# Kernel tuning notes

Measured on AMD Instinct MI355X. Metric: run time of the kernel, lower is better.

Reference implementation:

```python
import jax, jax.numpy as jnp
import numpy as np

HEADS = 12
DIM_HEAD = 64
SCALE = DIM_HEAD ** -0.5


def _layer_norm(x, w):
    # LayerNorm with learned weight and zero bias (bias is a frozen zeros buffer)
    mu = jnp.mean(x, axis=-1, keepdims=True)
    var = jnp.var(x, axis=-1, keepdims=True)
    return (x - mu) * jax.lax.rsqrt(var + 1e-5) * w


def setup_inputs() -> dict:
    key = jax.random.key(0)
    ks = jax.random.split(key, 6)
    b, n, j, dim = 4, 2048, 2048, 768
    inner = HEADS * DIM_HEAD  # 768
    return {
        "x": jax.random.normal(ks[0], (b, n, dim), dtype=jnp.float32),
        "context": jax.random.normal(ks[1], (b, j, dim), dtype=jnp.float32),
        "mask": jnp.zeros((b, n, j), dtype=jnp.float32),
        "ln_w": jnp.ones((dim,), dtype=jnp.float32),
        "Wq": jax.random.normal(ks[2], (dim, inner), dtype=jnp.float32) * (dim ** -0.5),
        "Wkv": jax.random.normal(ks[3], (dim, 2 * DIM_HEAD), dtype=jnp.float32) * (dim ** -0.5),
        "Wo": jax.random.normal(ks[4], (inner, dim), dtype=jnp.float32) * (inner ** -0.5),
    }


def reference(x, context, mask, ln_w, Wq, Wkv, Wo):
    b, n, dim = x.shape
    xn = _layer_norm(x, ln_w)
    # context_norm is Identity (norm_context=False)
    q = xn @ Wq  # [b, n, h*d]
    q = q.reshape(b, n, HEADS, DIM_HEAD).transpose(0, 2, 1, 3) * SCALE  # [b,h,n,d]
    kv = context @ Wkv  # [b, j, 2d]
    k, v = jnp.split(kv, 2, axis=-1)  # each [b, j, d] (multi-query: shared K/V)
    sim = jnp.einsum('bhid,bjd->bhij', q, k) + mask[:, None, :, :]
    # softmax with max-subtraction (jax.nn.softmax is max-stabilized, same math)
    attn = jax.nn.softmax(sim, axis=-1)
    out = jnp.einsum('bhij,bjd->bhid', attn, v)
    out = out.transpose(0, 2, 1, 3).reshape(b, n, HEADS * DIM_HEAD)
    out = out @ Wo
    # ff is None (parallel_ff=False)
    return out
```

## Files before the change

### kernel.cpp

```cpp
#include <hip/hip_runtime.h>


typedef unsigned short u16;
typedef unsigned int u32;
typedef __attribute__((ext_vector_type(8))) short short8;
typedef __attribute__((ext_vector_type(4))) short short4v;
typedef __attribute__((ext_vector_type(4))) float f32x4;
typedef __attribute__((ext_vector_type(2))) u32 u32x2;

#define L2E 1.44269504088896340736f

__device__ __forceinline__ u16 f2bf(float f) {
  u32 u = __float_as_uint(f);
  u += 0x7FFFu + ((u >> 16) & 1u);
  return (u16)(u >> 16);
}
__device__ __forceinline__ f32x4 mfma16(short8 a, short8 b, f32x4 c) {
  return __builtin_amdgcn_mfma_f32_16x16x32_bf16(a, b, c, 0, 0, 0);
}
__device__ __forceinline__ f32x4 mfma16k16(short4v a, short4v b, f32x4 c) {
  return __builtin_amdgcn_mfma_f32_16x16x16bf16_1k(a, b, c, 0, 0, 0);
}
__device__ __forceinline__ void gl2lds16(const u16* g, u16* s) {
  __builtin_amdgcn_global_load_lds(
      (const __attribute__((address_space(1))) u32*)g,
      (__attribute__((address_space(3))) u32*)s, 16, 0, 0);
}
__device__ __forceinline__ u32 pk2bf(float a, float b) {
  return ((__float_as_uint(a) + 0x8000u) >> 16) |
         ((__float_as_uint(b) + 0x8000u) & 0xffff0000u);
}

__device__ __forceinline__ void wt_tile(const float* in, u16* out, int K,
                                        int N, int tn, int tk,
                                        u16 (*tile)[72]) {
  const int t = threadIdx.x;
  const int tn0 = tn * 64, tk0 = tk * 64;
#pragma unroll
  for (int p = 0; p < 16; p++) {
    int e = p * 256 + t;
    int k = e >> 6, n = e & 63;
    tile[n][k] = f2bf(in[(size_t)(tk0 + k) * N + tn0 + n]);
  }
  __syncthreads();
#pragma unroll
  for (int p = 0; p < 16; p++) {
    int e = p * 256 + t;
    int n = e >> 6, k = e & 63;
    out[(size_t)(tn0 + n) * K + tk0 + k] = tile[n][k];
  }
}

__global__ __launch_bounds__(256)
void prep_kernel(const float* __restrict__ Wq, const float* __restrict__ Wkv,
                 const float* __restrict__ Wo, const float* __restrict__ ctx,
                 const float* __restrict__ x, const float* __restrict__ lnw,
                 u16* __restrict__ WqT, u16* __restrict__ WkvT,
                 u16* __restrict__ WoT, u16* __restrict__ ctxb,
                 u16* __restrict__ xn) {
  __shared__ u16 tile[64][72];
  __shared__ float red[8];
  __shared__ float sh_mu, sh_rs;
  const int bid = blockIdx.x, t = threadIdx.x;
  if (bid < 288) {
    const float* in = bid < 144 ? Wq : Wo;
    u16* out = bid < 144 ? WqT : WoT;
    int id = bid < 144 ? bid : bid - 144;
    wt_tile(in, out, 768, 768, id % 12, id / 12, tile);
  } else if (bid < 312) {
    int id = bid - 288;
    wt_tile(Wkv, WkvT, 768, 128, id % 2, id / 2, tile);
  } else if (bid < 6456) {
    int i = (bid - 312) * 256 + t;
    float4 v = ((const float4*)ctx)[i];
    ushort4 o;
    o.x = f2bf(v.x); o.y = f2bf(v.y); o.z = f2bf(v.z); o.w = f2bf(v.w);
    ((ushort4*)ctxb)[i] = o;
  } else {
    const int row = bid - 6456;
    const float* xr = x + (size_t)row * 768;
    float v0 = xr[t], v1 = xr[t + 256], v2 = xr[t + 512];
    float s = v0 + v1 + v2;
    float q = v0 * v0 + v1 * v1 + v2 * v2;
#pragma unroll
    for (int off = 32; off; off >>= 1) {
      s += __shfl_down(s, off);
      q += __shfl_down(q, off);
    }
    int wv = t >> 6;
    if ((t & 63) == 0) { red[wv * 2] = s; red[wv * 2 + 1] = q; }
    __syncthreads();
    if (t == 0) {
      float S = red[0] + red[2] + red[4] + red[6];
      float Q = red[1] + red[3] + red[5] + red[7];
      float mu = S * (1.0f / 768.0f);
      float var = Q * (1.0f / 768.0f) - mu * mu;
      sh_mu = mu;
      sh_rs = rsqrtf(var + 1e-5f);
    }
    __syncthreads();
    float mu = sh_mu, rs = sh_rs;
    u16* o = xn + (size_t)row * 768;
    o[t]       = f2bf((v0 - mu) * rs * lnw[t]);
    o[t + 256] = f2bf((v1 - mu) * rs * lnw[t + 256]);
    o[t + 512] = f2bf((v2 - mu) * rs * lnw[t + 512]);
  }
}

template <int BM, int BN>
__device__ __forceinline__ void gemm_stage(const u16* A, const u16* Bt, int K,
                                           int m0, int n0, int k0, u16* As,
                                           u16* Bs, int w, int l) {
  constexpr int CHA = BM * 8;
  constexpr int ISS = (BM + BN) * 8 / 256;
#pragma unroll
  for (int i = 0; i < ISS; i++) {
    const int c0 = (i * 4 + w) * 64;
    const int c = c0 + l;
    if (c0 < CHA) {
      int row = c >> 3, cc = c & 7, gc = cc ^ (row & 7);
      gl2lds16(A + (size_t)(m0 + row) * K + k0 + gc * 8, As + c0 * 8);
    } else {
      int cb = c - CHA;
      int row = cb >> 3, cc = cb & 7, gc = cc ^ (row & 7);
      gl2lds16(Bt + (size_t)(n0 + row) * K + k0 + gc * 8, Bs + (c0 - CHA) * 8);
    }
  }
}

template <int BM, int BN>
__device__ __forceinline__ void gemm_core(u16* As0, u16* As1, u16* Bs0,
                                          u16* Bs1, const u16* A,
                                          const u16* Bt, void* C, int N, int K,
                                          float scale, int out_bf16, int bx,
                                          int by) {
  constexpr int MT = BM / 32, NT = BN / 32;
  const int t = threadIdx.x;
  const int w = t >> 6, l = t & 63, lg = l >> 4, lc = l & 15;
  const int wm = w & 1, wn = w >> 1;
  const int n0 = bx * BN, m0 = by * BM;
  u16* Asb[2] = {As0, As1};
  u16* Bsb[2] = {Bs0, Bs1};

  f32x4 acc[MT][NT];
#pragma unroll
  for (int mt = 0; mt < MT; mt++)
#pragma unroll
    for (int nt = 0; nt < NT; nt++) acc[mt][nt] = (f32x4){0.f, 0.f, 0.f, 0.f};

  gemm_stage<BM, BN>(A, Bt, K, m0, n0, 0, As0, Bs0, w, l);
  int p = 0;
  for (int k0 = 0; k0 < K; k0 += 64, p ^= 1) {
    __syncthreads();
    if (k0 + 64 < K)
      gemm_stage<BM, BN>(A, Bt, K, m0, n0, k0 + 64, Asb[p ^ 1], Bsb[p ^ 1], w, l);
    const u16* As = Asb[p];
    const u16* Bs = Bsb[p];
#pragma unroll
    for (int ks = 0; ks < 2; ks++) {
      short8 af[MT], bfr[NT];
#pragma unroll
      for (int mt = 0; mt < MT; mt++) {
        int m = wm * (BM / 2) + mt * 16 + lc;
        af[mt] = *(const short8*)&As[m * 64 + (((ks * 4 + lg) ^ (m & 7)) * 8)];
      }
#pragma unroll
      for (int nt = 0; nt < NT; nt++) {
        int n = wn * (BN / 2) + nt * 16 + lc;
        bfr[nt] = *(const short8*)&Bs[n * 64 + (((ks * 4 + lg) ^ (n & 7)) * 8)];
      }
#pragma unroll
      for (int mt = 0; mt < MT; mt++)
#pragma unroll
        for (int nt = 0; nt < NT; nt++)
          acc[mt][nt] = mfma16(af[mt], bfr[nt], acc[mt][nt]);
    }
  }

#pragma unroll
  for (int mt = 0; mt < MT; mt++)
#pragma unroll
    for (int nt = 0; nt < NT; nt++)
#pragma unroll
      for (int r = 0; r < 4; r++) {
        int row = m0 + wm * (BM / 2) + mt * 16 + lg * 4 + r;
        int col = n0 + wn * (BN / 2) + nt * 16 + lc;
        float v = acc[mt][nt][r] * scale;
        if (out_bf16)
          ((u16*)C)[(size_t)row * N + col] = f2bf(v);
        else
          ((float*)C)[(size_t)row * N + col] = v;
      }
}

__global__ __launch_bounds__(256)
void gemm_qkv_kernel(const u16* __restrict__ xn, const u16* __restrict__ WqT,
                     u16* __restrict__ qb, const u16* __restrict__ ctxb,
                     const u16* __restrict__ WkvT, u16* __restrict__ kvb) {
  __shared__ __align__(16) u16 As[2][128 * 64];
  __shared__ __align__(16) u16 Bs[2][64 * 64];
  if (blockIdx.x < 12)
    gemm_core<128, 64>(As[0], As[1], Bs[0], Bs[1], xn, WqT, qb, 768, 768,
                       0.125f * L2E, 1, blockIdx.x, blockIdx.y);
  else
    gemm_core<128, 64>(As[0], As[1], Bs[0], Bs[1], ctxb, WkvT, kvb, 128, 768,
                       1.0f, 1, blockIdx.x - 12, blockIdx.y);
}

__global__ __launch_bounds__(256)
void gemm_o_kernel(const u16* __restrict__ aob, const u16* __restrict__ WoT,
                   float* __restrict__ out) {
  __shared__ __align__(16) u16 As[2][128 * 64];
  __shared__ __align__(16) u16 Bs[2][64 * 64];
  gemm_core<128, 64>(As[0], As[1], Bs[0], Bs[1], aob, WoT, out, 768, 768, 1.0f,
                     0, blockIdx.x, blockIdx.y);
}

__global__ void tv_kernel(const u16* __restrict__ kv, u16* __restrict__ vT) {
  __shared__ u16 tile[64][72];
  const int t = threadIdx.x;
  const int bb = blockIdx.y, j0 = blockIdx.x << 6;
#pragma unroll
  for (int p = 0; p < 16; p++) {
    int e = p * 256 + t;
    int j = e >> 6, d = e & 63;
    tile[j][d] = kv[(size_t)(bb * 2048 + j0 + j) * 128 + 64 + d];
  }
  __syncthreads();
#pragma unroll
  for (int p = 0; p < 16; p++) {
    int e = p * 256 + t;
    int d = e >> 6, j = e & 63;
    vT[(size_t)(bb * 64 + d) * 2048 + j0 + j] = tile[j][d];
  }
}

__device__ __forceinline__ void attn_stage(const u16* kvb, const u16* vtb,
                                           u16* Kq, u16* Vq, int j0, int w,
                                           int l) {
#pragma unroll
  for (int i = 0; i < 2; i++) {
    int c = i * 64 + l;
    int row = c >> 3, cc = c & 7, gc = cc ^ (row & 7);
    gl2lds16(kvb + (size_t)(j0 + w * 16 + row) * 128 + gc * 8,
             Kq + i * 64 * 8);
  }
#pragma unroll
  for (int i = 0; i < 2; i++) {
    int c = i * 64 + l;
    int d = c >> 1, hf = c & 1;
    gl2lds16(vtb + (size_t)d * 2048 + j0 + w * 16 + hf * 8, Vq + i * 64 * 8);
  }
}

__global__ __launch_bounds__(256, 3)
void attn_kernel(const u16* __restrict__ q, const u16* __restrict__ kv,
                 const u16* __restrict__ vT, const float* __restrict__ mask,
                 u16* __restrict__ ao) {
  __shared__ __align__(16) u16 lds[2][4][2048];

  const int t = threadIdx.x;
  const int i0 = blockIdx.x << 4;
  const int bb = blockIdx.y;
  const int hg = blockIdx.z;
  const int w = t >> 6, l = t & 63, lg = l >> 4, lc = l & 15;

  short8 qf[4][2];
#pragma unroll
  for (int hh = 0; hh < 4; hh++) {
    const int h = hg * 4 + hh;
    const u16* qp = q + (size_t)(bb * 2048 + i0 + lc) * 768 + h * 64 + lg * 8;
    qf[hh][0] = *(const short8*)qp;
    qf[hh][1] = *(const short8*)(qp + 32);
  }

  f32x4 o[4][4];
  float lsum[4] = {0.f, 0.f, 0.f, 0.f};
#pragma unroll
  for (int hh = 0; hh < 4; hh++)
#pragma unroll
    for (int nt = 0; nt < 4; nt++) o[hh][nt] = (f32x4){0.f, 0.f, 0.f, 0.f};

  const u16* kvb = kv + (size_t)bb * 2048 * 128;
  const u16* vtb = vT + (size_t)bb * 64 * 2048;
  const float* mrow =
      mask + (size_t)(bb * 2048 + i0 + lc) * 2048 + w * 16 + lg * 4;

  attn_stage(kvb, vtb, &lds[0][w][0], &lds[0][w][1024], 0, w, l);
  float4 mk = *(const float4*)mrow;

  for (int jj = 0; jj < 32; jj++) {
    const int p = jj & 1;
    __syncthreads();
    float4 mk_n = mk;
    if (jj + 1 < 32) {
      attn_stage(kvb, vtb, &lds[p ^ 1][w][0], &lds[p ^ 1][w][1024],
                 (jj + 1) * 64, w, l);
      mk_n = *(const float4*)(mrow + (jj + 1) * 64);
    }
    const u16* Kq = &lds[p][w][0];
    const u16* Vq = &lds[p][w][1024];
    short8 kf0 = *(const short8*)&Kq[lc * 64 + ((lg ^ (lc & 7)) * 8)];
    short8 kf1 = *(const short8*)&Kq[lc * 64 + (((4 + lg) ^ (lc & 7)) * 8)];
    short4v vfr[4];
#pragma unroll
    for (int nt = 0; nt < 4; nt++)
      vfr[nt] = *(const short4v*)&Vq[(nt * 16 + lc) * 16 + lg * 4];

#pragma unroll
    for (int hh = 0; hh < 4; hh++) {
      f32x4 s = mfma16(kf0, qf[hh][0], (f32x4){0.f, 0.f, 0.f, 0.f});
      s = mfma16(kf1, qf[hh][1], s);
      float p0 = __builtin_amdgcn_exp2f(__builtin_fmaf(mk.x, L2E, s[0]));
      float p1 = __builtin_amdgcn_exp2f(__builtin_fmaf(mk.y, L2E, s[1]));
      float p2 = __builtin_amdgcn_exp2f(__builtin_fmaf(mk.z, L2E, s[2]));
      float p3 = __builtin_amdgcn_exp2f(__builtin_fmaf(mk.w, L2E, s[3]));
      lsum[hh] += (p0 + p1) + (p2 + p3);
      u32x2 pp = {pk2bf(p0, p1), pk2bf(p2, p3)};
      short4v pk = __builtin_bit_cast(short4v, pp);
#pragma unroll
      for (int nt = 0; nt < 4; nt++)
        o[hh][nt] = mfma16k16(pk, vfr[nt], o[hh][nt]);
    }
    mk = mk_n;
  }

  float* f = (float*)&lds[0][0][0];
  const int ei = t >> 4, eg = t & 15;
#pragma unroll
  for (int hh = 0; hh < 4; hh++) {
    float lt = lsum[hh];
    lt += __shfl_xor(lt, 16);
    lt += __shfl_xor(lt, 32);
    __syncthreads();
    if (lg == 0) f[4096 + w * 16 + lc] = lt;
#pragma unroll
    for (int nt = 0; nt < 4; nt++)
#pragma unroll
      for (int r = 0; r < 4; r++)
        f[w * 1024 + (lg * 4 + r) * 64 + nt * 16 + lc] = o[hh][nt][r];
    __syncthreads();
    f32x4 sum = *(const f32x4*)&f[ei * 64 + eg * 4];
#pragma unroll
    for (int ww = 1; ww < 4; ww++) {
      f32x4 v2 = *(const f32x4*)&f[ww * 1024 + ei * 64 + eg * 4];
      sum[0] += v2[0]; sum[1] += v2[1]; sum[2] += v2[2]; sum[3] += v2[3];
    }
    float ltot = f[4096 + ei] + f[4096 + 16 + ei] + f[4096 + 32 + ei] +
                 f[4096 + 48 + ei];
    float inv = 1.0f / ltot;
    ushort4 ov;
    ov.x = f2bf(sum[0] * inv);
    ov.y = f2bf(sum[1] * inv);
    ov.z = f2bf(sum[2] * inv);
    ov.w = f2bf(sum[3] * inv);
    const int h = hg * 4 + hh;
    *(ushort4*)&ao[(size_t)(bb * 2048 + i0 + ei) * 768 + h * 64 + eg * 4] = ov;
  }
}

extern "C" void kernel_launch(void* const* d_in, const int* in_sizes, int n_in,
                              void* d_out, int out_size, void* d_ws,
                              size_t ws_size, hipStream_t stream) {
  const float* x    = (const float*)d_in[0];
  const float* ctx  = (const float*)d_in[1];
  const float* mask = (const float*)d_in[2];
  const float* lnw  = (const float*)d_in[3];
  const float* Wq   = (const float*)d_in[4];
  const float* Wkv  = (const float*)d_in[5];
  const float* Wo   = (const float*)d_in[6];

  char* ws = (char*)d_ws;
  u16* WqT  = (u16*)(ws + 0);
  u16* WkvT = (u16*)(ws + 1179648);
  u16* WoT  = (u16*)(ws + 1376256);
  u16* xn   = (u16*)(ws + 2555904);
  u16* ctxb = (u16*)(ws + 15138816);
  u16* qb   = (u16*)(ws + 27721728);
  u16* kvb  = (u16*)(ws + 40304640);
  u16* vTb  = (u16*)(ws + 42401792);
  u16* aob  = (u16*)(ws + 43450368);

  hipLaunchKernelGGL(prep_kernel, dim3(14648), dim3(256), 0, stream,
                     Wq, Wkv, Wo, ctx, x, lnw, WqT, WkvT, WoT, ctxb, xn);
  hipLaunchKernelGGL(gemm_qkv_kernel, dim3(14, 64), dim3(256), 0, stream,
                     xn, WqT, qb, ctxb, WkvT, kvb);
  hipLaunchKernelGGL(tv_kernel, dim3(32, 4), dim3(256), 0, stream, kvb, vTb);
  hipLaunchKernelGGL(attn_kernel, dim3(128, 4, 3), dim3(256), 0, stream,
                     qb, kvb, vTb, mask, aob);
  hipLaunchKernelGGL(gemm_o_kernel, dim3(12, 64), dim3(256), 0, stream,
                     aob, WoT, (float*)d_out);
}
```

Measured before the change: 289.2 us.

## Fuse V transpose into KV GEMM epilogue and load K/V directly from global

Removes the separate V-transpose kernel by having the KV GEMM epilogue write V transposed as well. The attention kernel drops its LDS double-buffered K/V staging and block-wide syncs, loading K and V fragments straight from global memory (served by cache) into registers. It also replaces the bf16 packing with a single byte-permute, which truncates instead of rounding, and hoists the mask scaling out of the head loop. In exchange, global loads now sit exposed inside the loop with no prefetch, and the transposed V stores from the GEMM are uncoalesced.

```diff
diff --git a/kernel.cpp b/kernel.cpp
--- a/kernel.cpp
+++ b/kernel.cpp
@@ -27,8 +27,8 @@
       (__attribute__((address_space(3))) u32*)s, 16, 0, 0);
 }
 __device__ __forceinline__ u32 pk2bf(float a, float b) {
-  return ((__float_as_uint(a) + 0x8000u) >> 16) |
-         ((__float_as_uint(b) + 0x8000u) & 0xffff0000u);
+  return __builtin_amdgcn_perm(__float_as_uint(b), __float_as_uint(a),
+                               0x07060302u);
 }
 
 __device__ __forceinline__ void wt_tile(const float* in, u16* out, int K,
@@ -133,7 +133,7 @@
                                           u16* Bs1, const u16* A,
                                           const u16* Bt, void* C, int N, int K,
                                           float scale, int out_bf16, int bx,
-                                          int by) {
+                                          int by, u16* vTout) {
   constexpr int MT = BM / 32, NT = BN / 32;
   const int t = threadIdx.x;
   const int w = t >> 6, l = t & 63, lg = l >> 4, lc = l & 15;
@@ -190,21 +190,26 @@
           ((u16*)C)[(size_t)row * N + col] = f2bf(v);
         else
           ((float*)C)[(size_t)row * N + col] = v;
+        if (vTout && col >= 64) {
+          int bbv = row >> 11, jv = row & 2047;
+          vTout[(size_t)(bbv * 64 + (col - 64)) * 2048 + jv] = f2bf(v);
+        }
       }
 }
 
 __global__ __launch_bounds__(256)
 void gemm_qkv_kernel(const u16* __restrict__ xn, const u16* __restrict__ WqT,
                      u16* __restrict__ qb, const u16* __restrict__ ctxb,
-                     const u16* __restrict__ WkvT, u16* __restrict__ kvb) {
+                     const u16* __restrict__ WkvT, u16* __restrict__ kvb,
+                     u16* __restrict__ vTb) {
   __shared__ __align__(16) u16 As[2][128 * 64];
   __shared__ __align__(16) u16 Bs[2][64 * 64];
   if (blockIdx.x < 12)
     gemm_core<128, 64>(As[0], As[1], Bs[0], Bs[1], xn, WqT, qb, 768, 768,
-                       0.125f * L2E, 1, blockIdx.x, blockIdx.y);
+                       0.125f * L2E, 1, blockIdx.x, blockIdx.y, nullptr);
   else
     gemm_core<128, 64>(As[0], As[1], Bs[0], Bs[1], ctxb, WkvT, kvb, 128, 768,
-                       1.0f, 1, blockIdx.x - 12, blockIdx.y);
+                       1.0f, 1, blockIdx.x - 12, blockIdx.y, vTb);
 }
 
 __global__ __launch_bounds__(256)
@@ -213,51 +218,14 @@
   __shared__ __align__(16) u16 As[2][128 * 64];
   __shared__ __align__(16) u16 Bs[2][64 * 64];
   gemm_core<128, 64>(As[0], As[1], Bs[0], Bs[1], aob, WoT, out, 768, 768, 1.0f,
-                     0, blockIdx.x, blockIdx.y);
-}
-
-__global__ void tv_kernel(const u16* __restrict__ kv, u16* __restrict__ vT) {
-  __shared__ u16 tile[64][72];
-  const int t = threadIdx.x;
-  const int bb = blockIdx.y, j0 = blockIdx.x << 6;
-#pragma unroll
-  for (int p = 0; p < 16; p++) {
-    int e = p * 256 + t;
-    int j = e >> 6, d = e & 63;
-    tile[j][d] = kv[(size_t)(bb * 2048 + j0 + j) * 128 + 64 + d];
-  }
-  __syncthreads();
-#pragma unroll
-  for (int p = 0; p < 16; p++) {
-    int e = p * 256 + t;
-    int d = e >> 6, j = e & 63;
-    vT[(size_t)(bb * 64 + d) * 2048 + j0 + j] = tile[j][d];
-  }
-}
-
-__device__ __forceinline__ void attn_stage(const u16* kvb, const u16* vtb,
-                                           u16* Kq, u16* Vq, int j0, int w,
-                                           int l) {
-#pragma unroll
-  for (int i = 0; i < 2; i++) {
-    int c = i * 64 + l;
-    int row = c >> 3, cc = c & 7, gc = cc ^ (row & 7);
-    gl2lds16(kvb + (size_t)(j0 + w * 16 + row) * 128 + gc * 8,
-             Kq + i * 64 * 8);
-  }
-#pragma unroll
-  for (int i = 0; i < 2; i++) {
-    int c = i * 64 + l;
-    int d = c >> 1, hf = c & 1;
-    gl2lds16(vtb + (size_t)d * 2048 + j0 + w * 16 + hf * 8, Vq + i * 64 * 8);
-  }
+                     0, blockIdx.x, blockIdx.y, nullptr);
 }
 
 __global__ __launch_bounds__(256, 3)
 void attn_kernel(const u16* __restrict__ q, const u16* __restrict__ kv,
                  const u16* __restrict__ vT, const float* __restrict__ mask,
                  u16* __restrict__ ao) {
-  __shared__ __align__(16) u16 lds[2][4][2048];
+  __shared__ float f[4160];
 
   const int t = threadIdx.x;
   const int i0 = blockIdx.x << 4;
@@ -268,8 +236,8 @@
   short8 qf[4][2];
 #pragma unroll
   for (int hh = 0; hh < 4; hh++) {
-    const int h = hg * 4 + hh;
-    const u16* qp = q + (size_t)(bb * 2048 + i0 + lc) * 768 + h * 64 + lg * 8;
+    const u16* qp =
+        q + (size_t)(bb * 2048 + i0 + lc) * 768 + (hg * 4 + hh) * 64 + lg * 8;
     qf[hh][0] = *(const short8*)qp;
     qf[hh][1] = *(const short8*)(qp + 32);
   }
@@ -281,40 +249,32 @@
 #pragma unroll
     for (int nt = 0; nt < 4; nt++) o[hh][nt] = (f32x4){0.f, 0.f, 0.f, 0.f};
 
-  const u16* kvb = kv + (size_t)bb * 2048 * 128;
-  const u16* vtb = vT + (size_t)bb * 64 * 2048;
+  const u16* kp = kv + (size_t)(bb * 2048 + w * 16 + lc) * 128 + lg * 8;
+  const u16* vp = vT + (size_t)(bb * 64 + lc) * 2048 + w * 16 + lg * 4;
   const float* mrow =
       mask + (size_t)(bb * 2048 + i0 + lc) * 2048 + w * 16 + lg * 4;
 
-  attn_stage(kvb, vtb, &lds[0][w][0], &lds[0][w][1024], 0, w, l);
   float4 mk = *(const float4*)mrow;
-
   for (int jj = 0; jj < 32; jj++) {
-    const int p = jj & 1;
-    __syncthreads();
+    short8 kf0 = *(const short8*)kp;
+    short8 kf1 = *(const short8*)(kp + 32);
+    short4v vfr[4];
+#pragma unroll
+    for (int nt = 0; nt < 4; nt++)
+      vfr[nt] = *(const short4v*)(vp + (size_t)nt * 16 * 2048);
     float4 mk_n = mk;
-    if (jj + 1 < 32) {
-      attn_stage(kvb, vtb, &lds[p ^ 1][w][0], &lds[p ^ 1][w][1024],
-                 (jj + 1) * 64, w, l);
-      mk_n = *(const float4*)(mrow + (jj + 1) * 64);
-    }
-    const u16* Kq = &lds[p][w][0];
-    const u16* Vq = &lds[p][w][1024];
-    short8 kf0 = *(const short8*)&Kq[lc * 64 + ((lg ^ (lc & 7)) * 8)];
-    short8 kf1 = *(const short8*)&Kq[lc * 64 + (((4 + lg) ^ (lc & 7)) * 8)];
-    short4v vfr[4];
-#pragma unroll
-    for (int nt = 0; nt < 4; nt++)
-      vfr[nt] = *(const short4v*)&Vq[(nt * 16 + lc) * 16 + lg * 4];
+    if (jj + 1 < 32) mk_n = *(const float4*)(mrow + (jj + 1) * 64);
+    float mkl0 = mk.x * L2E, mkl1 = mk.y * L2E;
+    float mkl2 = mk.z * L2E, mkl3 = mk.w * L2E;
 
 #pragma unroll
     for (int hh = 0; hh < 4; hh++) {
       f32x4 s = mfma16(kf0, qf[hh][0], (f32x4){0.f, 0.f, 0.f, 0.f});
       s = mfma16(kf1, qf[hh][1], s);
-      float p0 = __builtin_amdgcn_exp2f(__builtin_fmaf(mk.x, L2E, s[0]));
-      float p1 = __builtin_amdgcn_exp2f(__builtin_fmaf(mk.y, L2E, s[1]));
-      float p2 = __builtin_amdgcn_exp2f(__builtin_fmaf(mk.z, L2E, s[2]));
-      float p3 = __builtin_amdgcn_exp2f(__builtin_fmaf(mk.w, L2E, s[3]));
+      float p0 = __builtin_amdgcn_exp2f(s[0] + mkl0);
+      float p1 = __builtin_amdgcn_exp2f(s[1] + mkl1);
+      float p2 = __builtin_amdgcn_exp2f(s[2] + mkl2);
+      float p3 = __builtin_amdgcn_exp2f(s[3] + mkl3);
       lsum[hh] += (p0 + p1) + (p2 + p3);
       u32x2 pp = {pk2bf(p0, p1), pk2bf(p2, p3)};
       short4v pk = __builtin_bit_cast(short4v, pp);
@@ -322,10 +282,11 @@
       for (int nt = 0; nt < 4; nt++)
         o[hh][nt] = mfma16k16(pk, vfr[nt], o[hh][nt]);
     }
+    kp += 64 * 128;
+    vp += 64;
     mk = mk_n;
   }
 
-  float* f = (float*)&lds[0][0][0];
   const int ei = t >> 4, eg = t & 15;
 #pragma unroll
   for (int hh = 0; hh < 4; hh++) {
@@ -384,8 +345,7 @@
   hipLaunchKernelGGL(prep_kernel, dim3(14648), dim3(256), 0, stream,
                      Wq, Wkv, Wo, ctx, x, lnw, WqT, WkvT, WoT, ctxb, xn);
   hipLaunchKernelGGL(gemm_qkv_kernel, dim3(14, 64), dim3(256), 0, stream,
-                     xn, WqT, qb, ctxb, WkvT, kvb);
-  hipLaunchKernelGGL(tv_kernel, dim3(32, 4), dim3(256), 0, stream, kvb, vTb);
+                     xn, WqT, qb, ctxb, WkvT, kvb, vTb);
   hipLaunchKernelGGL(attn_kernel, dim3(128, 4, 3), dim3(256), 0, stream,
                      qb, kvb, vTb, mask, aob);
   hipLaunchKernelGGL(gemm_o_kernel, dim3(12, 64), dim3(256), 0, stream,
```

After: 363.2 us. +25.6%, slower.
